# Kernel optimization log

Measured on AMD Instinct MI355X. Metric: run time of the kernel, lower is better.

## Reference

```python
import jax, jax.numpy as jnp
import numpy as np

B, L, S = 128, 80, 8          # dialogues, utterances per dialogue, speakers
NODE_DIM, HIDDEN, HEADS, OUT_DIM = 768, 512, 8, 256
N = B * L


def _build_edges():
    """Replicates InterSentenceGNN.build_graph + Batch.from_data_list offsets."""
    rel = np.zeros((N, 3), np.float32)
    all_e, last = [], []
    eye3 = np.eye(3, dtype=np.float32)
    for b in range(B):
        off = b * L
        u = L - 1
        e, t = [], []
        for i in range(L):
            if i > 0:
                e += [[i - 1, i], [i, i - 1]]; t += [0, 0]   # REL_SEQ
            if i < u:
                e += [[i, u], [u, i]]; t += [1, 1]           # REL_CTX
        for s in range(S):                                   # REL_SPK, round-robin speakers
            g = list(range(s, L, S))
            for a in range(len(g)):
                for c in range(a + 1, len(g)):
                    e += [[g[a], g[c]], [g[c], g[a]]]; t += [2, 2]
        e = np.asarray(e, np.int64); t = np.asarray(t, np.int64)
        np.add.at(rel, e[:, 0] + off, eye3[t])               # out-degree per relation (pre-unique)
        all_e.append(np.unique(e, axis=0) + off)             # torch.unique(idx, dim=1)
        last.append(off + u)
    edge_index = np.concatenate(all_e, 0).T.astype(np.int32)  # [2, E], row0=src, row1=dst
    return edge_index, rel, np.asarray(last, np.int32)


def setup_inputs() -> dict:
    key = jax.random.key(0)
    ks = jax.random.split(key, 16)
    edge_index, rel_feat, last_idx = _build_edges()
    g = lambda k, shp, fan: jax.random.normal(k, shp, jnp.float32) * (1.0 / np.sqrt(fan))
    return {
        "x": jax.random.normal(ks[0], (N, NODE_DIM), jnp.float32),
        "rel_feat": jnp.asarray(rel_feat),
        "w1": g(ks[1], (3, 64), 3), "b1": jnp.zeros((64,), jnp.float32),
        "w2": g(ks[2], (64, 1), 64), "b2": jnp.zeros((1,), jnp.float32),
        "Wl1": g(ks[3], (NODE_DIM, HIDDEN), NODE_DIM), "bl1": jnp.zeros((HIDDEN,), jnp.float32),
        "Wr1": g(ks[4], (NODE_DIM, HIDDEN), NODE_DIM), "br1": jnp.zeros((HIDDEN,), jnp.float32),
        "att1": g(ks[5], (HEADS, HIDDEN // HEADS), HIDDEN // HEADS),
        "bias1": jnp.zeros((HIDDEN,), jnp.float32),
        "Wl2": g(ks[6], (HIDDEN, OUT_DIM), HIDDEN), "bl2": jnp.zeros((OUT_DIM,), jnp.float32),
        "Wr2": g(ks[7], (HIDDEN, OUT_DIM), HIDDEN), "br2": jnp.zeros((OUT_DIM,), jnp.float32),
        "att2": g(ks[8], (1, OUT_DIM), OUT_DIM),
        "bias2": jnp.zeros((OUT_DIM,), jnp.float32),
        "ln_g": jnp.ones((OUT_DIM,), jnp.float32), "ln_b": jnp.zeros((OUT_DIM,), jnp.float32),
        "edge_index": jnp.asarray(edge_index),
        "last_idx": jnp.asarray(last_idx),
    }


def _gatv2(x, Wl, bl, Wr, br, att, bias, src, dst, heads, ch, concat):
    """PyG GATv2Conv (eval mode, self-loops already in src/dst)."""
    n = x.shape[0]
    xl = (x @ Wl + bl).reshape(n, heads, ch)   # source transform (messages)
    xr = (x @ Wr + br).reshape(n, heads, ch)   # target transform
    e = jax.nn.leaky_relu(xl[src] + xr[dst], negative_slope=0.2)  # [E,H,C]
    logit = jnp.einsum("ehc,hc->eh", e, att)                      # [E,H]
    m = jax.ops.segment_max(logit, dst, num_segments=n)
    a = jnp.exp(logit - m[dst])
    denom = jax.ops.segment_sum(a, dst, num_segments=n)
    alpha = a / denom[dst]                                        # segment softmax over dst
    msg = (xl[src] * alpha[:, :, None]).reshape(-1, heads * ch)
    out = jax.ops.segment_sum(msg, dst, num_segments=n).reshape(n, heads, ch)
    out = out.reshape(n, heads * ch) if concat else out.mean(axis=1)
    return out + bias


def reference(x, rel_feat, w1, b1, w2, b2, Wl1, bl1, Wr1, br1, att1, bias1,
              Wl2, bl2, Wr2, br2, att2, bias2, ln_g, ln_b, edge_index, last_idx):
    n = x.shape[0]
    loops = jnp.arange(n, dtype=edge_index.dtype)
    src = jnp.concatenate([edge_index[0], loops])  # add_self_loops=True (PyG default)
    dst = jnp.concatenate([edge_index[1], loops])
    w = jax.nn.sigmoid(jax.nn.relu(rel_feat @ w1 + b1) @ w2 + b2)  # [N,1] node gate
    h = x * w
    h = jax.nn.elu(_gatv2(h, Wl1, bl1, Wr1, br1, att1, bias1, src, dst, HEADS, HIDDEN // HEADS, True))
    h = _gatv2(h, Wl2, bl2, Wr2, br2, att2, bias2, src, dst, 1, OUT_DIM, False)
    mu = jnp.mean(h, axis=-1, keepdims=True)
    var = jnp.mean((h - mu) ** 2, axis=-1, keepdims=True)
    h = (h - mu) * jax.lax.rsqrt(var + 1e-5) * ln_g + ln_b
    return h[last_idx]  # x[batch.ptr[1:] - 1]: last (context) node per dialogue
```

## Files before the change

### kernel.cpp

```cpp
#include <hip/hip_runtime.h>
#include <hip/hip_bf16.h>

#define NN 10240
#define LL 80
#define BB 128

typedef _Float16 half8 __attribute__((ext_vector_type(8)));
typedef _Float16 half2v __attribute__((ext_vector_type(2)));
typedef float f32x4 __attribute__((ext_vector_type(4)));

#define GLD16(gptr, lptr)                                                        \
  __builtin_amdgcn_global_load_lds(                                              \
      (const __attribute__((address_space(1))) void*)(gptr),                     \
      (__attribute__((address_space(3))) void*)(lptr), 16, 0, 0)

__device__ __forceinline__ float dot2f(half2v a, half2v b, float c) {
#if __has_builtin(__builtin_amdgcn_fdot2)
  return __builtin_amdgcn_fdot2(a, b, c, false);
#else
  return c + (float)a.x * (float)b.x + (float)a.y * (float)b.y;
#endif
}
__device__ __forceinline__ half2v u2h(unsigned int u) { half2v r; __builtin_memcpy(&r, &u, 4); return r; }
__device__ __forceinline__ unsigned int h2u(half2v h) { unsigned int u; __builtin_memcpy(&u, &h, 4); return u; }
__device__ __forceinline__ int roff(int r) { return r * 72; }

__device__ __forceinline__ float dotq4r(uint4 a, uint4 b, const half2v* atv, int qb, float acc) {
  const half2v c02 = {(_Float16)0.2f, (_Float16)0.2f};
  unsigned int aa[4] = {a.x, a.y, a.z, a.w};
  unsigned int bb[4] = {b.x, b.y, b.z, b.w};
#pragma unroll
  for (int j = 0; j < 4; ++j) {
    half2v e = u2h(aa[j]) + u2h(bb[j]);
    half2v l = __builtin_elementwise_max(e, e * c02);
    acc = dot2f(l, atv[qb + j], acc);
  }
  return acc;
}

__global__ __launch_bounds__(256) void prep_all(
    const float* __restrict__ x, const float* __restrict__ rel,
    const float* __restrict__ w1, const float* __restrict__ b1,
    const float* __restrict__ w2, const float* __restrict__ b2,
    const float* __restrict__ Wl1, const float* __restrict__ Wr1,
    const float* __restrict__ Wl2, const float* __restrict__ Wr2,
    const float* __restrict__ bl1, const float* __restrict__ br1,
    const float* __restrict__ att1,
    _Float16* __restrict__ h0, _Float16* __restrict__ Wt1,
    _Float16* __restrict__ Wt2cat,
    float* __restrict__ biasc, _Float16* __restrict__ att_h) {
  __shared__ float tile[32][33];
  int bid = blockIdx.x;
  int tid = threadIdx.x;
  if (bid < 2560) {
    int wave = tid >> 6, l = tid & 63;
    int n = bid * 4 + wave;
    float r0 = rel[n * 3 + 0], r1 = rel[n * 3 + 1], r2 = rel[n * 3 + 2];
    float v = r0 * w1[l] + r1 * w1[64 + l] + r2 * w1[128 + l] + b1[l];
    v = v > 0.f ? v : 0.f;
    v *= w2[l];
    for (int d = 32; d; d >>= 1) v += __shfl_down(v, d, 64);
    float s = __shfl(v, 0, 64);
    float g = 1.f / (1.f + __expf(-(s + b2[0])));
    const float4* xr = (const float4*)(x + (size_t)n * 768);
    _Float16* hr = h0 + (size_t)n * 768;
#pragma unroll
    for (int i = 0; i < 3; ++i) {
      int f = i * 64 + l;
      float4 xv = xr[f];
      half2v p0 = {(_Float16)(xv.x * g), (_Float16)(xv.y * g)};
      half2v p1 = {(_Float16)(xv.z * g), (_Float16)(xv.w * g)};
      uint2 ov = {h2u(p0), h2u(p1)};
      *(uint2*)&hr[f * 4] = ov;
    }
    return;
  }
  int r = bid - 2560;
  const float* W;
  _Float16* Wt;
  int K, Nc, bx, by;
  if (r < 384)      { W = Wl1; Wt = Wt1;                          K = 768; Nc = 512; bx = r % 16;       by = r / 16; }
  else if (r < 768) { W = Wr1; Wt = Wt1 + (size_t)512 * 768;      K = 768; Nc = 512; bx = (r-384) % 16; by = (r-384) / 16; }
  else if (r < 896) { W = Wl2; Wt = Wt2cat;                       K = 512; Nc = 256; bx = (r-768) % 8;  by = (r-768) / 8; }
  else if (r < 1024){ W = Wr2; Wt = Wt2cat + (size_t)256 * 512;   K = 512; Nc = 256; bx = (r-896) % 8;  by = (r-896) / 8; }
  else {
    for (int i = tid; i < 1024; i += 256) biasc[i] = (i < 512) ? bl1[i] : br1[i - 512];
    for (int i = tid; i < 512; i += 256) att_h[i] = (_Float16)att1[i];
    return;
  }
  int n0 = bx * 32, k0 = by * 32;
  int c = tid & 31, rr = tid >> 5;
#pragma unroll
  for (int p = 0; p < 4; ++p) {
    int rw = p * 8 + rr;
    tile[rw][c] = W[(size_t)(k0 + rw) * Nc + n0 + c];
  }
  __syncthreads();
#pragma unroll
  for (int p = 0; p < 4; ++p) {
    int rw = p * 8 + rr;
    Wt[(size_t)(n0 + rw) * K + k0 + c] = (_Float16)tile[c][rw];
  }
}

__global__ __launch_bounds__(512, 6) void gemm1gat1(
    const _Float16* __restrict__ h0, const _Float16* __restrict__ Wt1,
    const float* __restrict__ biasc, const _Float16* __restrict__ att_h,
    const float* __restrict__ bias1, _Float16* __restrict__ h1) {
  __shared__ __align__(16) char smem[53248];
  _Float16* Ab = (_Float16*)smem;
  _Float16* Bb = (_Float16*)(smem + 20480);
  _Float16* s_xl = (_Float16*)smem;
  _Float16* s_xr = (_Float16*)(smem + 11520);
  float* s_logit = (float*)(smem + 23040);
  signed char* s_src8 = (signed char*)(smem + 27200);
  float* s_hub = (float*)(smem + 28240);
  _Float16* s_xlT = (_Float16*)(smem + 28560);
  _Float16* s_P = (_Float16*)smem;

  int bx = blockIdx.x;
  int h = bx >> 7, b = bx & 127;
  int base = b * LL;
  int tid = threadIdx.x;
  int wave = tid >> 6, lane = tid & 63;
  int lr = lane & 15, lk = lane >> 4;

  int segA8 = ((lane & 7) ^ ((lane >> 3) & 7)) * 8;
  int r0a = wave * 16 + (lane >> 3);
  const _Float16* aP0 = h0;
  const _Float16* aP1 = h0;
  if (wave < 5) {
    aP0 = h0 + (size_t)(base + r0a) * 768 + segA8;
    aP1 = h0 + (size_t)(base + r0a + 8) * 768 + segA8;
  }
  int rb0 = r0a, rb1 = r0a + 8;
  int wr0 = (rb0 < 64) ? (h * 64 + rb0) : (512 + h * 64 + (rb0 - 64));
  int wr1 = (rb1 < 64) ? (h * 64 + rb1) : (512 + h * 64 + (rb1 - 64));
  const _Float16* bP0 = Wt1 + (size_t)wr0 * 768 + segA8;
  const _Float16* bP1 = Wt1 + (size_t)wr1 * 768 + segA8;

  f32x4 acc[5] = {};
  if (wave < 5) {
    GLD16(aP0, Ab + wave * 1024);
    GLD16(aP1, Ab + wave * 1024 + 512);
  }
  GLD16(bP0, Bb + wave * 1024);
  GLD16(bP1, Bb + wave * 1024 + 512);
  __syncthreads();
  for (int t = 0; t < 12; ++t) {
    int cur = t & 1;
    if (t < 11) {
      int k0 = (t + 1) * 64;
      int nb = cur ^ 1;
      if (wave < 5) {
        GLD16(aP0 + k0, Ab + nb * 5120 + wave * 1024);
        GLD16(aP1 + k0, Ab + nb * 5120 + wave * 1024 + 512);
      }
      GLD16(bP0 + k0, Bb + nb * 8192 + wave * 1024);
      GLD16(bP1 + k0, Bb + nb * 8192 + wave * 1024 + 512);
    }
    const _Float16* Ac = Ab + cur * 5120;
    const _Float16* Bc = Bb + cur * 8192;
    int rB = wave * 16 + lr;
#pragma unroll
    for (int s2 = 0; s2 < 2; ++s2) {
      int cx = ((s2 * 4 + lk) ^ (lr & 7)) * 8;
      half8 bf = *(const half8*)(Bc + rB * 64 + cx);
#pragma unroll
      for (int m = 0; m < 5; ++m) {
        half8 af = *(const half8*)(Ac + (m * 16 + lr) * 64 + cx);
        acc[m] = __builtin_amdgcn_mfma_f32_16x16x32_f16(af, bf, acc[m], 0, 0, 0);
      }
    }
    __syncthreads();
  }
  {
    int c = wave * 16 + lr;
    bool isxl = c < 64;
    int cc = isxl ? c : c - 64;
    float bb = biasc[(isxl ? 0 : 512) + h * 64 + cc];
    _Float16* dst = isxl ? s_xl : s_xr;
#pragma unroll
    for (int m = 0; m < 5; ++m)
#pragma unroll
      for (int rg = 0; rg < 4; ++rg) {
        int row = m * 16 + lk * 4 + rg;
        _Float16 hv = (_Float16)(acc[m][rg] + bb);
        dst[roff(row) + cc] = hv;
        if (isxl) s_xlT[cc * 88 + row] = hv;
      }
  }
  if (tid < 79) {
    int d = tid;
    signed char list[13];
    int c = 0;
    list[c++] = (signed char)d;
    if (d > 0) list[c++] = (signed char)(d - 1);
    if (d + 1 < 79) list[c++] = (signed char)(d + 1);
    list[c++] = 79;
    for (int j = d & 7; j < 80; j += 8)
      if (j != d && j != 79) list[c++] = (signed char)j;
    for (int i = c; i < 13; ++i) list[i] = -1;
#pragma unroll
    for (int i = 0; i < 13; ++i) s_src8[i * 80 + d] = list[i];
  }
  __syncthreads();

  const unsigned int* pat = (const unsigned int*)(att_h + h * 64);
  half2v atv[32];
#pragma unroll
  for (int q = 0; q < 32; ++q) atv[q] = u2h(__builtin_amdgcn_readfirstlane(pat[q]));
  if (tid < 474) {
    int d = tid / 6, io = tid % 6;
    const uint4* pxr = (const uint4*)(s_xr + roff(d));
    uint4 xrr[8];
#pragma unroll
    for (int q = 0; q < 8; ++q) xrr[q] = pxr[q];
#pragma unroll
    for (int k = 0; k < 3; ++k) {
      int i = io + 6 * k;
      if (i < 13) {
        int src = s_src8[i * 80 + d];
        if (src < 0) {
          s_logit[i * 80 + d] = -3e38f;
        } else {
          const uint4* pxl = (const uint4*)(s_xl + roff(src));
          float a2 = 0.f;
#pragma unroll
          for (int q = 0; q < 8; ++q) a2 = dotq4r(pxl[q], xrr[q], atv, q * 4, a2);
          s_logit[i * 80 + d] = a2;
        }
      }
    }
  } else {
    int j = tid - 474;
    const uint4* pxr = (const uint4*)(s_xr + roff(79));
    uint4 xrr[8];
#pragma unroll
    for (int q = 0; q < 8; ++q) xrr[q] = pxr[q];
#pragma unroll
    for (int k = 0; k < 3; ++k) {
      int s = j + 38 * k;
      if (s < 80) {
        const uint4* pxl = (const uint4*)(s_xl + roff(s));
        float a2 = 0.f;
#pragma unroll
        for (int q = 0; q < 8; ++q) a2 = dotq4r(pxl[q], xrr[q], atv, q * 4, a2);
        s_hub[s] = a2;
      }
    }
  }
  __syncthreads();

  {
    uint4 z4 = {0u, 0u, 0u, 0u};
    for (int z = tid; z < 1040; z += 512) ((uint4*)smem)[z] = z4;
  }
  float va[13], inv_d = 0.f;
  bool isd = tid < 79;
  if (isd) {
    int d = tid;
    float m = -3e38f;
#pragma unroll
    for (int i = 0; i < 13; ++i) { va[i] = s_logit[i * 80 + d]; m = fmaxf(m, va[i]); }
    float sum = 0.f;
#pragma unroll
    for (int i = 0; i < 13; ++i) { va[i] = __expf(va[i] - m); sum += va[i]; }
    inv_d = 1.f / sum;
  }
  float he0 = 0.f, he1 = 0.f, hinv = 0.f;
  if (wave == 7) {
    int l = lane;
    float v0 = s_hub[l];
    float v1 = (l < 16) ? s_hub[64 + l] : -3e38f;
    float m = fmaxf(v0, v1);
    for (int d = 32; d; d >>= 1) m = fmaxf(m, __shfl_xor(m, d, 64));
    he0 = __expf(v0 - m);
    he1 = (l < 16) ? __expf(v1 - m) : 0.f;
    float sum = he0 + he1;
    for (int d = 32; d; d >>= 1) sum += __shfl_xor(sum, d, 64);
    hinv = 1.f / sum;
  }
  __syncthreads();

  if (isd) {
    int d = tid;
#pragma unroll
    for (int i = 0; i < 13; ++i) {
      int src = s_src8[i * 80 + d];
      if (src >= 0) s_P[d * 104 + src] = (_Float16)(va[i] * inv_d);
    }
  }
  if (wave == 7) {
    int l = lane;
    s_P[79 * 104 + l] = (_Float16)(he0 * hinv);
    if (l < 16) s_P[79 * 104 + 64 + l] = (_Float16)(he1 * hinv);
  }
  __syncthreads();

  {
    int nt = (wave < 4) ? 3 : 2;
    int tb = (wave < 4) ? wave * 3 : 12 + (wave - 4) * 2;
    for (int tt = 0; tt < nt; ++tt) {
      int t = tb + tt;
      int m = t >> 2, n = t & 3;
      f32x4 a = {};
#pragma unroll
      for (int kc = 0; kc < 3; ++kc) {
        half8 af = *(const half8*)(s_P + (m * 16 + lr) * 104 + kc * 32 + lk * 8);
        half8 bf = *(const half8*)(s_xlT + (n * 16 + lr) * 88 + kc * 32 + lk * 8);
        a = __builtin_amdgcn_mfma_f32_16x16x32_f16(af, bf, a, 0, 0, 0);
      }
      int c = n * 16 + lr;
      float bb = bias1[h * 64 + c];
#pragma unroll
      for (int rg = 0; rg < 4; ++rg) {
        int d = m * 16 + lk * 4 + rg;
        float v = a[rg] + bb;
        v = v > 0.f ? v : __expf(v) - 1.f;
        h1[(size_t)(base + d) * 512 + h * 64 + c] = (_Float16)v;
      }
    }
  }
}

__global__ __launch_bounds__(256) void gemm2a(
    const _Float16* __restrict__ h1, const _Float16* __restrict__ Bt,
    const float* __restrict__ bl2, const float* __restrict__ br2,
    _Float16* __restrict__ xl2, _Float16* __restrict__ xr2) {
  __shared__ __align__(16) char smem[16384];
  _Float16* Ab = (_Float16*)smem;
  _Float16* Bb = (_Float16*)(smem + 8192);
  int bx = blockIdx.x;
  bool isxr = bx >= 640;
  int bl = isxr ? bx - 640 : bx;
  int mb = bl >> 2, nb = bl & 3;
  int tid = threadIdx.x;
  int wave = tid >> 6, lane = tid & 63;
  int lr = lane & 15, lk = lane >> 4;
  int seg8 = ((lane & 3) ^ ((lane >> 3) & 3)) * 8;
  int row = tid >> 2;
  size_t arow = isxr ? ((size_t)(mb * 64 + row) * 80 + 79) : (size_t)(mb * 64 + row);
  const _Float16* aP = h1 + arow * 512 + seg8;
  const _Float16* bP = Bt + (size_t)((isxr ? 256 : 0) + nb * 64 + row) * 512 + seg8;
  int xk8 = (lk ^ ((lr >> 1) & 3)) * 8;
  f32x4 acc[4] = {};
  GLD16(aP, Ab + wave * 512);
  GLD16(bP, Bb + wave * 512);
  __syncthreads();
  for (int t = 0; t < 16; ++t) {
    int cur = t & 1;
    if (t < 15) {
      int k0 = (t + 1) * 32;
      int nbuf = cur ^ 1;
      GLD16(aP + k0, Ab + nbuf * 2048 + wave * 512);
      GLD16(bP + k0, Bb + nbuf * 2048 + wave * 512);
    }
    const _Float16* Ac = Ab + cur * 2048;
    const _Float16* Bc = Bb + cur * 2048;
    half8 bf = *(const half8*)(Bc + (wave * 16 + lr) * 32 + xk8);
#pragma unroll
    for (int m = 0; m < 4; ++m) {
      half8 af = *(const half8*)(Ac + (m * 16 + lr) * 32 + xk8);
      acc[m] = __builtin_amdgcn_mfma_f32_16x16x32_f16(af, bf, acc[m], 0, 0, 0);
    }
    __syncthreads();
  }
  int col = nb * 64 + wave * 16 + lr;
  float bb = isxr ? br2[col] : bl2[col];
  _Float16* dst = isxr ? xr2 : xl2;
#pragma unroll
  for (int m = 0; m < 4; ++m)
#pragma unroll
    for (int rg = 0; rg < 4; ++rg) {
      int r = mb * 64 + m * 16 + lk * 4 + rg;
      dst[(size_t)r * 256 + col] = (_Float16)(acc[m][rg] + bb);
    }
}

#define PX 264
__global__ __launch_bounds__(512) void gat2ln(
    const _Float16* __restrict__ xl2, const _Float16* __restrict__ xr2,
    const float* __restrict__ att2, const float* __restrict__ bias2,
    const float* __restrict__ ln_g, const float* __restrict__ ln_b,
    float* __restrict__ out) {
  __shared__ __align__(16) _Float16 s_x[80 * PX];
  __shared__ _Float16 s_att[256];
  __shared__ _Float16 s_xr[256];
  __shared__ float s_red[80];
  __shared__ float s_sum[4], s_sq[4];

  int b = blockIdx.x;
  int tid = threadIdx.x;
  int wave = tid >> 6, lane = tid & 63;

  if (tid < 256) s_att[tid] = (_Float16)att2[tid];
  if (tid >= 256 && tid < 512 - 0) {  }
  for (int t = tid; t < 2560; t += 512) {
    int row = t >> 5, q = t & 31;
    uint4 v = *(const uint4*)(xl2 + ((size_t)(b * 80 + row)) * 256 + q * 8);
    *(uint4*)(s_x + row * PX + q * 8) = v;
  }
  if (tid < 256) s_xr[tid] = xr2[(size_t)b * 256 + tid];
  __syncthreads();
  if (tid < 160) {
    int r = tid >> 1, hf = tid & 1;
    const half2v* xa = (const half2v*)(s_x + r * PX + hf * 128);
    const half2v* xr = (const half2v*)(s_xr + hf * 128);
    const half2v* at = (const half2v*)(s_att + hf * 128);
    float lg = 0.f;
    const half2v c02 = {(_Float16)0.2f, (_Float16)0.2f};
#pragma unroll
    for (int q = 0; q < 64; ++q) {
      half2v e = xa[q] + xr[q];
      half2v l = __builtin_elementwise_max(e, e * c02);
      lg = dot2f(l, at[q], lg);
    }
    lg += __shfl_xor(lg, 1, 64);
    if (hf == 0) s_red[r] = lg;
  }
  __syncthreads();
  if (wave == 7) {
    float v0 = s_red[lane];
    float v1 = (lane < 16) ? s_red[64 + lane] : -3e38f;
    float m = fmaxf(v0, v1);
    for (int d = 32; d; d >>= 1) m = fmaxf(m, __shfl_xor(m, d, 64));
    float e0 = __expf(v0 - m);
    float e1 = (lane < 16) ? __expf(v1 - m) : 0.f;
    float sum = e0 + e1;
    for (int d = 32; d; d >>= 1) sum += __shfl_xor(sum, d, 64);
    float inv = 1.f / sum;
    s_red[lane] = e0 * inv;
    if (lane < 16) s_red[64 + lane] = e1 * inv;
  }
  __syncthreads();
  float v = 0.f;
  if (tid < 256) {
    float a = 0.f;
#pragma unroll
    for (int r = 0; r < 80; ++r) a += s_red[r] * (float)s_x[r * PX + tid];
    v = a + bias2[tid];
    float p = v;
    for (int d = 32; d; d >>= 1) p += __shfl_down(p, d, 64);
    if (lane == 0) s_sum[wave] = p;
    float q = v * v;
    for (int d = 32; d; d >>= 1) q += __shfl_down(q, d, 64);
    if (lane == 0) s_sq[wave] = q;
  }
  __syncthreads();
  if (tid < 256) {
    float mu = (s_sum[0] + s_sum[1] + s_sum[2] + s_sum[3]) * (1.f / 256.f);
    float ex2 = (s_sq[0] + s_sq[1] + s_sq[2] + s_sq[3]) * (1.f / 256.f);
    float var = ex2 - mu * mu;
    float r = rsqrtf(var + 1e-5f);
    out[b * 256 + tid] = (v - mu) * r * ln_g[tid] + ln_b[tid];
  }
}

extern "C" void kernel_launch(void* const* d_in, const int* in_sizes, int n_in,
                              void* d_out, int out_size, void* d_ws, size_t ws_size,
                              hipStream_t stream) {
  const float* x      = (const float*)d_in[0];
  const float* rel    = (const float*)d_in[1];
  const float* w1     = (const float*)d_in[2];
  const float* b1     = (const float*)d_in[3];
  const float* w2     = (const float*)d_in[4];
  const float* b2     = (const float*)d_in[5];
  const float* Wl1    = (const float*)d_in[6];
  const float* bl1    = (const float*)d_in[7];
  const float* Wr1    = (const float*)d_in[8];
  const float* br1    = (const float*)d_in[9];
  const float* att1   = (const float*)d_in[10];
  const float* bias1  = (const float*)d_in[11];
  const float* Wl2    = (const float*)d_in[12];
  const float* bl2    = (const float*)d_in[13];
  const float* Wr2    = (const float*)d_in[14];
  const float* br2    = (const float*)d_in[15];
  const float* att2   = (const float*)d_in[16];
  const float* bias2  = (const float*)d_in[17];
  const float* ln_g   = (const float*)d_in[18];
  const float* ln_b   = (const float*)d_in[19];
  float* out = (float*)d_out;

  char* p = (char*)d_ws;
  _Float16* h0     = (_Float16*)p; p += (size_t)NN * 768 * 2;
  _Float16* h1     = (_Float16*)p; p += (size_t)NN * 512 * 2;
  _Float16* Wt1    = (_Float16*)p; p += (size_t)1024 * 768 * 2;
  _Float16* Wt2cat = (_Float16*)p; p += (size_t)512 * 512 * 2;
  _Float16* att_h  = (_Float16*)p; p += 1024;
  float* biasc     = (float*)p; p += 1024 * 4;
  _Float16* xl2    = (_Float16*)p; p += (size_t)NN * 256 * 2;
  _Float16* xr2    = (_Float16*)p; p += (size_t)BB * 256 * 2;

  prep_all<<<2560 + 1025, 256, 0, stream>>>(x, rel, w1, b1, w2, b2, Wl1, Wr1, Wl2, Wr2,
                                            bl1, br1, att1, h0, Wt1, Wt2cat, biasc, att_h);

  gemm1gat1<<<1024, 512, 0, stream>>>(h0, Wt1, biasc, att_h, bias1, h1);

  gemm2a<<<648, 256, 0, stream>>>(h1, Wt2cat, bl2, br2, xl2, xr2);

  gat2ln<<<BB, 512, 0, stream>>>(xl2, xr2, att2, bias2, ln_g, ln_b, out);
}
```

Before: 168.2 us.

## Split GEMM K across wave pairs with 2 N-tiles per wave and LDS reduction

The first-layer GEMM now gives each wave two 16-column N tiles and only half of each 64-wide K slice. Waves 0-3 and 4-7 cover the two K halves, and their partial accumulators are summed through LDS scratch before the epilogue. This reuses each A fragment across two MFMAs and halves the A-fragment LDS reads per wave. It costs extra accumulator registers, a scratch round-trip with two more barriers, and it zero-pads the s_xlT tails. The epilogue now runs on only 4 waves.

Result: no change. 168.1 us (-0.1%).

```diff
diff --git a/kernel.cpp b/kernel.cpp
--- a/kernel.cpp
+++ b/kernel.cpp
@@ -139,7 +139,12 @@
   const _Float16* bP0 = Wt1 + (size_t)wr0 * 768 + segA8;
   const _Float16* bP1 = Wt1 + (size_t)wr1 * 768 + segA8;
 
-  f32x4 acc[5] = {};
+  int g2 = wave & 3, kh = wave >> 2;
+  int n0c = (2 * g2) * 16 + lr;
+  int n1c = (2 * g2 + 1) * 16 + lr;
+  int cx = ((kh * 4 + lk) ^ (lr & 7)) * 8;
+
+  f32x4 acc[5][2] = {};
   if (wave < 5) {
     GLD16(aP0, Ab + wave * 1024);
     GLD16(aP1, Ab + wave * 1024 + 512);
@@ -161,34 +166,60 @@
     }
     const _Float16* Ac = Ab + cur * 5120;
     const _Float16* Bc = Bb + cur * 8192;
-    int rB = wave * 16 + lr;
-#pragma unroll
-    for (int s2 = 0; s2 < 2; ++s2) {
-      int cx = ((s2 * 4 + lk) ^ (lr & 7)) * 8;
-      half8 bf = *(const half8*)(Bc + rB * 64 + cx);
-#pragma unroll
-      for (int m = 0; m < 5; ++m) {
-        half8 af = *(const half8*)(Ac + (m * 16 + lr) * 64 + cx);
-        acc[m] = __builtin_amdgcn_mfma_f32_16x16x32_f16(af, bf, acc[m], 0, 0, 0);
-      }
+    half8 bf0 = *(const half8*)(Bc + n0c * 64 + cx);
+    half8 bf1 = *(const half8*)(Bc + n1c * 64 + cx);
+#pragma unroll
+    for (int m = 0; m < 5; ++m) {
+      half8 af = *(const half8*)(Ac + (m * 16 + lr) * 64 + cx);
+      acc[m][0] = __builtin_amdgcn_mfma_f32_16x16x32_f16(af, bf0, acc[m][0], 0, 0, 0);
+      acc[m][1] = __builtin_amdgcn_mfma_f32_16x16x32_f16(af, bf1, acc[m][1], 0, 0, 0);
     }
     __syncthreads();
   }
   {
-    int c = wave * 16 + lr;
-    bool isxl = c < 64;
-    int cc = isxl ? c : c - 64;
-    float bb = biasc[(isxl ? 0 : 512) + h * 64 + cc];
-    _Float16* dst = isxl ? s_xl : s_xr;
-#pragma unroll
-    for (int m = 0; m < 5; ++m)
-#pragma unroll
-      for (int rg = 0; rg < 4; ++rg) {
-        int row = m * 16 + lk * 4 + rg;
-        _Float16 hv = (_Float16)(acc[m][rg] + bb);
-        dst[roff(row) + cc] = hv;
-        if (isxl) s_xlT[cc * 88 + row] = hv;
-      }
+    float* scr = (float*)smem;
+    if (wave >= 4) {
+      int bi = ((wave - 4) * 64 + lane) * 40;
+#pragma unroll
+      for (int m = 0; m < 5; ++m)
+#pragma unroll
+        for (int j = 0; j < 2; ++j)
+          *(f32x4*)(scr + bi + (m * 2 + j) * 4) = acc[m][j];
+    }
+    __syncthreads();
+    if (wave < 4) {
+      int bi = (wave * 64 + lane) * 40;
+#pragma unroll
+      for (int m = 0; m < 5; ++m)
+#pragma unroll
+        for (int j = 0; j < 2; ++j)
+          acc[m][j] += *(const f32x4*)(scr + bi + (m * 2 + j) * 4);
+    }
+    __syncthreads();
+  }
+  {
+    int z = tid;
+    if (z < 512) s_xlT[(z >> 3) * 88 + 80 + (z & 7)] = (_Float16)0.f;
+    if (z < 8) s_xlT[64 * 88 + z] = (_Float16)0.f;
+  }
+  if (wave < 4) {
+#pragma unroll
+    for (int j = 0; j < 2; ++j) {
+      int c = (wave * 2 + j) * 16 + lr;
+      bool isxl = c < 64;
+      int cc = isxl ? c : c - 64;
+      float bb = biasc[(isxl ? 0 : 512) + h * 64 + cc];
+      _Float16* dst = isxl ? s_xl : s_xr;
+#pragma unroll
+      for (int m = 0; m < 5; ++m)
+#pragma unroll
+        for (int rg = 0; rg < 4; ++rg) {
+          int row = m * 16 + lk * 4 + rg;
+          _Float16 hv = (_Float16)(acc[m][j][rg] + bb);
+          dst[roff(row) + cc] = hv;
+          if (isxl) s_xlT[cc * 88 + row] = hv;
+        }
+    }
   }
   if (tid < 79) {
     int d = tid;
@@ -395,7 +426,6 @@
   int wave = tid >> 6, lane = tid & 63;
 
   if (tid < 256) s_att[tid] = (_Float16)att2[tid];
-  if (tid >= 256 && tid < 512 - 0) {  }
   for (int t = tid; t < 2560; t += 512) {
     int row = t >> 5, q = t & 31;
     uint4 v = *(const uint4*)(xl2 + ((size_t)(b * 80 + row)) * 256 + q * 8);
```
